# Kernel optimization log

Hardware: AMD Instinct MI355X
Metric: run time of the kernel (lower is better)

Reference implementation:

```python
import jax, jax.numpy as jnp
import numpy as np

# config matching init_kwargs
C = 256; G = 16; GC = C // G; K = 3; P = K * K
PAD = 1; STR = 1; DIL = 1; OFFSET_SCALE = 1.0
N, H, W = 8, 64, 64


def setup_inputs() -> dict:
    key = jax.random.key(0)
    ks = jax.random.split(key, 8)
    def rn(k, shape, sc):
        return jax.random.normal(k, shape, jnp.float32) * sc
    return {
        "x": jax.random.normal(ks[0], (N, H, W, C), jnp.float32),
        "dw_w": rn(ks[1], (C, 1, K, K), 0.1),          # depthwise conv weight (OIHW, groups=C)
        "dw_b": jnp.zeros((C,), jnp.float32),
        "ln_g": jnp.ones((C,), jnp.float32),
        "ln_b": jnp.zeros((C,), jnp.float32),
        "off_w": rn(ks[2], (G * P * 2, C), 0.01),      # offset head (small so offsets stay sane)
        "off_b": jnp.zeros((G * P * 2,), jnp.float32),
        "mask_w": rn(ks[3], (G * P, C), 0.01),
        "mask_b": jnp.zeros((G * P,), jnp.float32),
        "in_w": rn(ks[4], (C, C), 0.05),
        "in_b": jnp.zeros((C,), jnp.float32),
        "out_w": rn(ks[5], (C, C), 0.05),
        "out_b": jnp.zeros((C,), jnp.float32),
    }


def _layer_norm(x, g, b, eps=1e-6):
    m = x.mean(-1, keepdims=True)
    v = ((x - m) ** 2).mean(-1, keepdims=True)
    return (x - m) * jax.lax.rsqrt(v + eps) * g + b


def _grid_sample_bilinear(img, grid):
    # img: (B, Cc, Hh, Ww); grid: (B, L, P, 2) normalized to [-1, 1], (x, y) order.
    # Matches torch.grid_sample(mode='bilinear', padding_mode='zeros', align_corners=False).
    B, Cc, Hh, Ww = img.shape
    gx = (grid[..., 0] + 1.0) * (Ww * 0.5) - 0.5
    gy = (grid[..., 1] + 1.0) * (Hh * 0.5) - 0.5
    x0 = jnp.floor(gx); y0 = jnp.floor(gy)
    tx = gx - x0; ty = gy - y0
    img_f = img.reshape(B, Cc, Hh * Ww)
    def corner(xi, yi, w):
        valid = (xi >= 0) & (xi < Ww) & (yi >= 0) & (yi < Hh)
        idx = (jnp.clip(yi, 0, Hh - 1) * Ww + jnp.clip(xi, 0, Ww - 1)).astype(jnp.int32)
        v = jnp.take_along_axis(img_f, idx.reshape(B, 1, -1), axis=2)  # (B, Cc, L*P)
        return v * (w * valid).reshape(B, 1, -1)
    out = (corner(x0, y0, (1 - tx) * (1 - ty)) + corner(x0 + 1, y0, tx * (1 - ty))
           + corner(x0, y0 + 1, (1 - tx) * ty) + corner(x0 + 1, y0 + 1, tx * ty))
    return out.reshape(B, Cc, grid.shape[1], grid.shape[2])  # (B, Cc, L, P)


def _dcnv3_core(x, offset, mask):
    # x: (N,H,W,C) value features; offset: (N,H,W,G*P*2); mask: (N,H,W,G*P)
    xpad = jnp.pad(x, ((0, 0), (PAD, PAD), (PAD, PAD), (0, 0)))
    Hi, Wi = H + 2 * PAD, W + 2 * PAD
    Ho, Wo = H, W
    # reference points (centers of receptive field), normalized by padded size
    start = (DIL * (K - 1)) // 2 + 0.5
    ry = (start + jnp.arange(Ho, dtype=jnp.float32) * STR) / Hi
    rx = (start + jnp.arange(Wo, dtype=jnp.float32) * STR) / Wi
    ref = jnp.stack([jnp.broadcast_to(rx[None, :], (Ho, Wo)),
                     jnp.broadcast_to(ry[:, None], (Ho, Wo))], -1)  # (Ho,Wo,2) (x,y)
    # dilation grid, x-major flattening to match torch meshgrid('ij') ordering
    d = jnp.arange(K, dtype=jnp.float32) * DIL - (DIL * (K - 1)) // 2
    kgrid = jnp.stack([jnp.repeat(d, K) / Wi, jnp.tile(d, K) / Hi], -1)  # (P,2)
    off = offset.reshape(N, Ho, Wo, G, P, 2)
    norm = jnp.array([Wi, Hi], jnp.float32)
    loc = (ref[None, :, :, None, None, :]
           + kgrid[None, None, None, None, :, :] * OFFSET_SCALE
           + off * OFFSET_SCALE / norm)                      # (N,Ho,Wo,G,P,2)
    sg = (2.0 * loc - 1.0).reshape(N, Ho * Wo, G, P, 2)
    sg = sg.transpose(0, 2, 1, 3, 4).reshape(N * G, Ho * Wo, P, 2)
    val = xpad.reshape(N, Hi * Wi, G * GC).transpose(0, 2, 1).reshape(N * G, GC, Hi, Wi)
    samp = _grid_sample_bilinear(val, sg)                    # (N*G, GC, Ho*Wo, P)
    m = mask.reshape(N, Ho * Wo, G, P).transpose(0, 2, 1, 3).reshape(N * G, 1, Ho * Wo, P)
    out = (samp * m).sum(-1)                                 # (N*G, GC, Ho*Wo)
    return out.reshape(N, G * GC, Ho * Wo).transpose(0, 2, 1).reshape(N, Ho, Wo, C)


def reference(x, dw_w, dw_b, ln_g, ln_b, off_w, off_b, mask_w, mask_b, in_w, in_b, out_w, out_b):
    xp = x @ in_w.T + in_b                                   # input_proj (values)
    # depthwise conv -> LN (channels_last) -> exact GELU
    y = jax.lax.conv_general_dilated(
        x.transpose(0, 3, 1, 2), dw_w, (1, 1), ((PAD, PAD), (PAD, PAD)),
        feature_group_count=C, dimension_numbers=('NCHW', 'OIHW', 'NCHW'))
    y = y + dw_b[None, :, None, None]
    x1 = jax.nn.gelu(_layer_norm(y.transpose(0, 2, 3, 1), ln_g, ln_b), approximate=False)
    offset = x1 @ off_w.T + off_b                            # (N,H,W,G*P*2)
    mlogits = (x1 @ mask_w.T + mask_b).reshape(N, H, W, G, P)
    mask = jax.nn.softmax(mlogits, axis=-1).reshape(N, H, W, G * P)
    out = _dcnv3_core(xp, offset, mask)
    return out @ out_w.T + out_b
```

## Files before the change

### kernel.cpp

```cpp
#include <hip/hip_runtime.h>


#define LL 32768
#define CC 256

typedef __bf16 bf16;
typedef __bf16 bf16x4 __attribute__((ext_vector_type(4)));
typedef __bf16 bf16x8 __attribute__((ext_vector_type(8)));
typedef float f32x4v __attribute__((ext_vector_type(4)));

__device__ __forceinline__ void gload16(const bf16* g, const bf16* lds_base) {
    __builtin_amdgcn_global_load_lds(
        (const __attribute__((address_space(1))) void*)g,
        (__attribute__((address_space(3))) void*)lds_base, 16, 0, 0);
}

__global__ __launch_bounds__(256) void k_prep(
    const float* __restrict__ in_w, const float* __restrict__ off_w,
    const float* __restrict__ mask_w, const float* __restrict__ out_w,
    const float* __restrict__ dw_w, const float* __restrict__ off_b,
    const float* __restrict__ mask_b,
    bf16* __restrict__ in_h, bf16* __restrict__ in_l,
    bf16* __restrict__ hw_h, bf16* __restrict__ hw_l,
    bf16* __restrict__ out_h, bf16* __restrict__ out_l,
    float* __restrict__ dwT, float* __restrict__ hbias) {
    int idx = blockIdx.x * 256 + threadIdx.x;
    if (idx < 60416) {
        const float* s; bf16 *hi, *lo; int i;
        if (idx < 16384)      { s = in_w;   hi = in_h;          lo = in_l;          i = idx; }
        else if (idx < 34816) { s = off_w;  hi = hw_h;          lo = hw_l;          i = idx - 16384; }
        else if (idx < 44032) { s = mask_w; hi = hw_h + 73728;  lo = hw_l + 73728;  i = idx - 34816; }
        else                  { s = out_w;  hi = out_h;         lo = out_l;         i = idx - 44032; }
        float4 v = *(const float4*)(s + (size_t)i * 4);
        bf16x4 h, l;
        h[0] = (bf16)v.x; l[0] = (bf16)(v.x - (float)h[0]);
        h[1] = (bf16)v.y; l[1] = (bf16)(v.y - (float)h[1]);
        h[2] = (bf16)v.z; l[2] = (bf16)(v.z - (float)h[2]);
        h[3] = (bf16)v.w; l[3] = (bf16)(v.w - (float)h[3]);
        *(bf16x4*)(hi + (size_t)i * 4) = h;
        *(bf16x4*)(lo + (size_t)i * 4) = l;
    } else if (idx < 62720) {
        int e = idx - 60416;
        int c = e & 255, j = e >> 8;
        dwT[j * 256 + c] = dw_w[c * 9 + j];
    } else if (idx < 63232) {
        int e = idx - 62720;
        hbias[e] = (e < 288) ? off_b[e] : (e < 432 ? mask_b[e - 288] : 0.f);
    } else if (idx < 68352) {
        int e = idx - 63232;
        bf16x4 z = {(bf16)0.f, (bf16)0.f, (bf16)0.f, (bf16)0.f};
        *(bf16x4*)(hw_h + 110592 + (size_t)e * 4) = z;
        *(bf16x4*)(hw_l + 110592 + (size_t)e * 4) = z;
    }
}

__global__ __launch_bounds__(256) void k_dwln(
    const float* __restrict__ x, const float* __restrict__ dwT,
    const float* __restrict__ dw_b, const float* __restrict__ ln_g,
    const float* __restrict__ ln_b, bf16* __restrict__ x1h,
    bf16* __restrict__ xb) {
    int t = threadIdx.x;
    int q = t >> 6, u = t & 63;
    int l = blockIdx.x * 4 + q;
    int w = l & 63, h = (l >> 6) & 63, n = l >> 12;
    int c0 = u * 4;

    float4 acc = *(const float4*)(dw_b + c0);
    float4 xc = {0.f, 0.f, 0.f, 0.f};
#pragma unroll
    for (int kh = 0; kh < 3; ++kh) {
        int hh = h + kh - 1;
        if (hh < 0 || hh >= 64) continue;
#pragma unroll
        for (int kw = 0; kw < 3; ++kw) {
            int ww = w + kw - 1;
            if (ww < 0 || ww >= 64) continue;
            float4 xv = *(const float4*)(x + (size_t)(((n * 64 + hh) * 64) + ww) * CC + c0);
            if (kh == 1 && kw == 1) xc = xv;
            float4 wv = *(const float4*)(dwT + (kh * 3 + kw) * 256 + c0);
            acc.x += xv.x * wv.x; acc.y += xv.y * wv.y;
            acc.z += xv.z * wv.z; acc.w += xv.w * wv.w;
        }
    }
    bf16x4 xcb;
    xcb[0] = (bf16)xc.x; xcb[1] = (bf16)xc.y;
    xcb[2] = (bf16)xc.z; xcb[3] = (bf16)xc.w;
    *(bf16x4*)(xb + (size_t)l * CC + c0) = xcb;

    float s = acc.x + acc.y + acc.z + acc.w;
    float ss = acc.x * acc.x + acc.y * acc.y + acc.z * acc.z + acc.w * acc.w;
#pragma unroll
    for (int d = 1; d < 64; d <<= 1) {
        s += __shfl_xor(s, d);
        ss += __shfl_xor(ss, d);
    }
    float mean = s * (1.0f / 256.0f);
    float var = ss * (1.0f / 256.0f) - mean * mean;
    float rstd = rsqrtf(var + 1e-6f);
    float4 gv = *(const float4*)(ln_g + c0);
    float4 bv = *(const float4*)(ln_b + c0);
    float xn0 = (acc.x - mean) * rstd * gv.x + bv.x;
    float xn1 = (acc.y - mean) * rstd * gv.y + bv.y;
    float xn2 = (acc.z - mean) * rstd * gv.z + bv.z;
    float xn3 = (acc.w - mean) * rstd * gv.w + bv.w;
    bf16x4 oh;
    oh[0] = (bf16)(0.5f * xn0 * (1.0f + erff(xn0 * 0.70710678118654752f)));
    oh[1] = (bf16)(0.5f * xn1 * (1.0f + erff(xn1 * 0.70710678118654752f)));
    oh[2] = (bf16)(0.5f * xn2 * (1.0f + erff(xn2 * 0.70710678118654752f)));
    oh[3] = (bf16)(0.5f * xn3 * (1.0f + erff(xn3 * 0.70710678118654752f)));
    *(bf16x4*)(x1h + (size_t)l * CC + c0) = oh;
}

template <bool OBF16>
__global__ __launch_bounds__(256) void k_gemm(
    const bf16* __restrict__ A, const bf16* __restrict__ Wh,
    const bf16* __restrict__ Wl, const float* __restrict__ bias,
    float* __restrict__ C32, bf16* __restrict__ Cbf, int Nout) {
    int mb = blockIdx.x * 128, nb = blockIdx.y * 128;
    int t = threadIdx.x, wave = t >> 6, lane = t & 63;
    int wm = wave & 1, wn = wave >> 1;
    int fm = lane & 15, fq = lane >> 4;

    __shared__ bf16 smem[12288];

    const bf16* gbase[6];
    const bf16* lbase[6];
#pragma unroll
    for (int j = 0; j < 6; ++j) {
        int seg = wave * 6 + j;
        int arr = seg >> 3;
        int row = (seg & 7) * 16 + (lane >> 2);
        int col = (lane & 3) * 8;
        const bf16* g = (arr == 0) ? (A + (size_t)(mb + row) * CC + col)
                      : (arr == 1) ? (Wh + (size_t)(nb + row) * CC + col)
                                   : (Wl + (size_t)(nb + row) * CC + col);
        gbase[j] = g;
        lbase[j] = smem + seg * 512;
    }

    f32x4v acc[4][4];
#pragma unroll
    for (int i = 0; i < 4; ++i)
#pragma unroll
        for (int j = 0; j < 4; ++j) acc[i][j] = (f32x4v){0.f, 0.f, 0.f, 0.f};

    for (int kc = 0; kc < 256; kc += 32) {
#pragma unroll
        for (int j = 0; j < 6; ++j) gload16(gbase[j] + kc, lbase[j]);
        __syncthreads();

        bf16x8 af[4], bfh[4], bfl[4];
#pragma unroll
        for (int i = 0; i < 4; ++i)
            af[i] = *(const bf16x8*)&smem[(wm * 64 + i * 16 + fm) * 32 + fq * 8];
#pragma unroll
        for (int j = 0; j < 4; ++j) {
            int br = wn * 64 + j * 16 + fm;
            bfh[j] = *(const bf16x8*)&smem[4096 + br * 32 + fq * 8];
            bfl[j] = *(const bf16x8*)&smem[8192 + br * 32 + fq * 8];
        }
#pragma unroll
        for (int i = 0; i < 4; ++i)
#pragma unroll
            for (int j = 0; j < 4; ++j) {
                acc[i][j] = __builtin_amdgcn_mfma_f32_16x16x32_bf16(
                    af[i], bfh[j], acc[i][j], 0, 0, 0);
                acc[i][j] = __builtin_amdgcn_mfma_f32_16x16x32_bf16(
                    af[i], bfl[j], acc[i][j], 0, 0, 0);
            }
        __syncthreads();
    }

#pragma unroll
    for (int j = 0; j < 4; ++j) {
        int n_g = nb + wn * 64 + j * 16 + fm;
        if (n_g >= Nout) continue;
        float bv = bias[n_g];
#pragma unroll
        for (int i = 0; i < 4; ++i) {
            int m_g = mb + wm * 64 + i * 16 + fq * 4;
#pragma unroll
            for (int rg = 0; rg < 4; ++rg) {
                float o = acc[i][j][rg] + bv;
                if (OBF16)
                    Cbf[(size_t)(m_g + rg) * Nout + n_g] = (bf16)o;
                else
                    C32[(size_t)(m_g + rg) * Nout + n_g] = o;
            }
        }
    }
}

__global__ __launch_bounds__(256) void k_gather(
    const bf16* __restrict__ xp, const bf16* __restrict__ head,
    bf16* __restrict__ rows) {
    int t = threadIdx.x;
    int q = t >> 5, u = t & 31;
    int l = blockIdx.x * 8 + q;
    int w = l & 63, h = (l >> 6) & 63, n = l >> 12;

    __shared__ float offs[8][288];
    __shared__ float ms[8][144];
    for (int j = u; j < 288; j += 32) offs[q][j] = (float)head[(size_t)l * 432 + j];
    for (int j = u; j < 144; j += 32) ms[q][j] = (float)head[(size_t)l * 432 + 288 + j];
    __syncthreads();

    if (u < 16) {
        int g = u;
        float mx = -1e30f;
#pragma unroll
        for (int p = 0; p < 9; ++p) mx = fmaxf(mx, ms[q][g * 9 + p]);
        float s = 0.f, e[9];
#pragma unroll
        for (int p = 0; p < 9; ++p) { e[p] = expf(ms[q][g * 9 + p] - mx); s += e[p]; }
        float inv = 1.0f / s;
#pragma unroll
        for (int p = 0; p < 9; ++p) ms[q][g * 9 + p] = e[p] * inv;
    }
    __syncthreads();

    int g = u >> 1;
    int c0 = g * 16 + (u & 1) * 8;
    const bf16* base = xp + (size_t)n * 4096 * CC + c0;
    float a0 = 0.f, a1 = 0.f, a2 = 0.f, a3 = 0.f;
    float a4 = 0.f, a5 = 0.f, a6 = 0.f, a7 = 0.f;
#pragma unroll
    for (int p = 0; p < 9; ++p) {
        float ox = offs[q][g * 18 + p * 2 + 0];
        float oy = offs[q][g * 18 + p * 2 + 1];
        float ax = (float)(w + (p / 3) - 1) + ox;
        float ay = (float)(h + (p % 3) - 1) + oy;
        float x0f = floorf(ax), y0f = floorf(ay);
        int x0 = (int)x0f, y0 = (int)y0f;
        float tx = ax - x0f, ty = ay - y0f;
        float m = ms[q][g * 9 + p];
        int idx[4]; float cw[4];
#pragma unroll
        for (int cr = 0; cr < 4; ++cr) {
            int xx = x0 + (cr & 1), yy = y0 + (cr >> 1);
            bool v = (xx >= 0) & (xx < 64) & (yy >= 0) & (yy < 64);
            int xc = min(max(xx, 0), 63), yc = min(max(yy, 0), 63);
            idx[cr] = (yc * 64 + xc) * CC;
            float wx = (cr & 1) ? tx : (1.f - tx);
            float wy = (cr >> 1) ? ty : (1.f - ty);
            cw[cr] = v ? (m * wx * wy) : 0.f;
        }
#pragma unroll
        for (int cr = 0; cr < 4; ++cr) {
            bf16x8 vb = *(const bf16x8*)(base + idx[cr]);
            float wt = cw[cr];
            a0 += wt * (float)vb[0]; a1 += wt * (float)vb[1];
            a2 += wt * (float)vb[2]; a3 += wt * (float)vb[3];
            a4 += wt * (float)vb[4]; a5 += wt * (float)vb[5];
            a6 += wt * (float)vb[6]; a7 += wt * (float)vb[7];
        }
    }
    bf16x8 oh;
    oh[0] = (bf16)a0; oh[1] = (bf16)a1; oh[2] = (bf16)a2; oh[3] = (bf16)a3;
    oh[4] = (bf16)a4; oh[5] = (bf16)a5; oh[6] = (bf16)a6; oh[7] = (bf16)a7;
    *(bf16x8*)(rows + (size_t)l * CC + c0) = oh;
}

__device__ __forceinline__ float dot256f(const float* a, const float* wrow) {
    const float4* w4 = (const float4*)wrow;
    float s = 0.f;
#pragma unroll 16
    for (int i = 0; i < 64; ++i) {
        float4 u = w4[i];
        const float* ap = a + i * 4;
        s += ap[0] * u.x + ap[1] * u.y + ap[2] * u.z + ap[3] * u.w;
    }
    return s;
}

__global__ __launch_bounds__(256) void k_inproj_fb(
    const float* __restrict__ x, const float* __restrict__ in_w,
    const float* __restrict__ in_b, float* __restrict__ xp) {
    int l = blockIdx.x;
    int t = threadIdx.x;
    __shared__ float xa[256];
    xa[t] = x[l * CC + t];
    __syncthreads();
    xp[l * CC + t] = dot256f(xa, in_w + t * CC) + in_b[t];
}

__device__ __forceinline__ float fetch_px_fb(const float* base, int yy, int xx) {
    if (xx < 0 || xx >= 64 || yy < 0 || yy >= 64) return 0.f;
    return base[(yy * 64 + xx) * CC];
}

__global__ __launch_bounds__(256) void k_main_fb(
    const float* __restrict__ x, const float* __restrict__ xp,
    const float* __restrict__ dw_w, const float* __restrict__ dw_b,
    const float* __restrict__ ln_g, const float* __restrict__ ln_b,
    const float* __restrict__ off_w, const float* __restrict__ off_b,
    const float* __restrict__ mask_w, const float* __restrict__ mask_b,
    const float* __restrict__ out_w, const float* __restrict__ out_b,
    float* __restrict__ out) {
    int l = blockIdx.x;
    int t = threadIdx.x;
    int w = l & 63, h = (l >> 6) & 63, n = l >> 12;
    __shared__ float x1[256];
    __shared__ float red[256];
    __shared__ float offs[288];
    __shared__ float ms[144];
    __shared__ float row[256];

    float acc = dw_b[t];
#pragma unroll
    for (int kh = 0; kh < 3; ++kh) {
        int hh = h + kh - 1;
        if (hh < 0 || hh >= 64) continue;
#pragma unroll
        for (int kw = 0; kw < 3; ++kw) {
            int ww = w + kw - 1;
            if (ww < 0 || ww >= 64) continue;
            acc += x[(((n * 64 + hh) * 64) + ww) * CC + t] * dw_w[t * 9 + kh * 3 + kw];
        }
    }
    red[t] = acc;
    __syncthreads();
    for (int s = 128; s > 0; s >>= 1) {
        if (t < s) red[t] += red[t + s];
        __syncthreads();
    }
    float mean = red[0] * (1.0f / 256.0f);
    __syncthreads();
    float d = acc - mean;
    red[t] = d * d;
    __syncthreads();
    for (int s = 128; s > 0; s >>= 1) {
        if (t < s) red[t] += red[t + s];
        __syncthreads();
    }
    float var = red[0] * (1.0f / 256.0f);
    float xn = d * rsqrtf(var + 1e-6f) * ln_g[t] + ln_b[t];
    x1[t] = 0.5f * xn * (1.0f + erff(xn * 0.70710678118654752f));
    __syncthreads();

    offs[t] = dot256f(x1, off_w + t * CC) + off_b[t];
    if (t < 32) {
        int j = 256 + t;
        offs[j] = dot256f(x1, off_w + j * CC) + off_b[j];
    }
    if (t < 144) ms[t] = dot256f(x1, mask_w + t * CC) + mask_b[t];
    __syncthreads();

    if (t < 16) {
        int g = t;
        float mx = -1e30f;
#pragma unroll
        for (int p = 0; p < 9; ++p) mx = fmaxf(mx, ms[g * 9 + p]);
        float s = 0.f, e[9];
#pragma unroll
        for (int p = 0; p < 9; ++p) { e[p] = expf(ms[g * 9 + p] - mx); s += e[p]; }
        float inv = 1.0f / s;
#pragma unroll
        for (int p = 0; p < 9; ++p) ms[g * 9 + p] = e[p] * inv;
    }
    __syncthreads();

    int g = t >> 4;
    const float* base = xp + (size_t)n * 64 * 64 * CC + t;
    float acc2 = 0.f;
#pragma unroll
    for (int p = 0; p < 9; ++p) {
        float ox = offs[g * 18 + p * 2 + 0];
        float oy = offs[g * 18 + p * 2 + 1];
        float ax = (float)(w + (p / 3) - 1) + ox;
        float ay = (float)(h + (p % 3) - 1) + oy;
        float x0f = floorf(ax), y0f = floorf(ay);
        int x0 = (int)x0f, y0 = (int)y0f;
        float tx = ax - x0f, ty = ay - y0f;
        float v00 = fetch_px_fb(base, y0, x0);
        float v01 = fetch_px_fb(base, y0, x0 + 1);
        float v10 = fetch_px_fb(base, y0 + 1, x0);
        float v11 = fetch_px_fb(base, y0 + 1, x0 + 1);
        float bl = (v00 * (1.f - tx) + v01 * tx) * (1.f - ty) +
                   (v10 * (1.f - tx) + v11 * tx) * ty;
        acc2 += ms[g * 9 + p] * bl;
    }
    row[t] = acc2;
    __syncthreads();
    out[l * CC + t] = dot256f(row, out_w + t * CC) + out_b[t];
}

extern "C" void kernel_launch(void* const* d_in, const int* in_sizes, int n_in,
                              void* d_out, int out_size, void* d_ws,
                              size_t ws_size, hipStream_t stream) {
    const float* x      = (const float*)d_in[0];
    const float* dw_w   = (const float*)d_in[1];
    const float* dw_b   = (const float*)d_in[2];
    const float* ln_g   = (const float*)d_in[3];
    const float* ln_b   = (const float*)d_in[4];
    const float* off_w  = (const float*)d_in[5];
    const float* off_b  = (const float*)d_in[6];
    const float* mask_w = (const float*)d_in[7];
    const float* mask_b = (const float*)d_in[8];
    const float* in_w   = (const float*)d_in[9];
    const float* in_b   = (const float*)d_in[10];
    const float* out_w  = (const float*)d_in[11];
    const float* out_b  = (const float*)d_in[12];
    float* out = (float*)d_out;

    const size_t szBF    = (size_t)LL * CC * 2;
    const size_t szHEADB = (size_t)LL * 432 * 2;
    const size_t szWB    = 1300480;
    const size_t need    = 3 * szBF + szHEADB + szWB;

    dim3 blk(256);
    if (ws_size >= need) {
        char* p = (char*)d_ws;
        bf16* x1h = (bf16*)p; p += szBF;
        bf16* xpb = (bf16*)p; p += szBF;
        bf16* xb  = (bf16*)p; p += szBF;
        bf16* headb = (bf16*)p; p += szHEADB;
        bf16* in_h  = (bf16*)p; p += 131072;
        bf16* in_l  = (bf16*)p; p += 131072;
        bf16* hw_h  = (bf16*)p; p += 262144;
        bf16* hw_l  = (bf16*)p; p += 262144;
        bf16* out_h = (bf16*)p; p += 131072;
        bf16* out_l = (bf16*)p; p += 131072;
        float* dwT  = (float*)p; p += 9216;
        float* hbias = (float*)p;
        bf16* rows = x1h;

        k_prep<<<dim3(267), blk, 0, stream>>>(in_w, off_w, mask_w, out_w, dw_w,
                                              off_b, mask_b, in_h, in_l, hw_h,
                                              hw_l, out_h, out_l, dwT, hbias);
        k_dwln<<<dim3(LL / 4), blk, 0, stream>>>(x, dwT, dw_b, ln_g, ln_b, x1h, xb);
        k_gemm<true><<<dim3(256, 2), blk, 0, stream>>>(
            xb, in_h, in_l, in_b, nullptr, xpb, 256);
        k_gemm<true><<<dim3(256, 4), blk, 0, stream>>>(
            x1h, hw_h, hw_l, hbias, nullptr, headb, 432);
        k_gather<<<dim3(LL / 8), blk, 0, stream>>>(xpb, headb, rows);
        k_gemm<false><<<dim3(256, 2), blk, 0, stream>>>(
            rows, out_h, out_l, out_b, out, nullptr, 256);
    } else {
        float* xp = (float*)d_ws;
        k_inproj_fb<<<dim3(LL), blk, 0, stream>>>(x, in_w, in_b, xp);
        k_main_fb<<<dim3(LL), blk, 0, stream>>>(x, xp, dw_w, dw_b, ln_g, ln_b,
                                                off_w, off_b, mask_w, mask_b,
                                                out_w, out_b, out);
    }
}
```

Before: 218.8 us.

## Drop low-part weight MFMA in input/head GEMMs and widen gather per thread

Adds a template flag so the input-projection and offset/mask head GEMMs use only the high bf16 part of the weights, which halves their MFMA work and their LDS/global loads. The output GEMM keeps the two-part split. The gather kernel is restructured: one thread now handles a full 16-channel group for one pixel, the bf16 head row is copied into LDS with vector loads, and the softmax is computed in registers, which removes a sync and the float staging. The risk is lower accuracy for offsets and values, since the residual bf16 correction term is gone.

```diff
diff --git a/kernel.cpp b/kernel.cpp
--- a/kernel.cpp
+++ b/kernel.cpp
@@ -111,7 +111,7 @@
     *(bf16x4*)(x1h + (size_t)l * CC + c0) = oh;
 }
 
-template <bool OBF16>
+template <bool OBF16, bool TWOP>
 __global__ __launch_bounds__(256) void k_gemm(
     const bf16* __restrict__ A, const bf16* __restrict__ Wh,
     const bf16* __restrict__ Wl, const float* __restrict__ bias,
@@ -121,13 +121,15 @@
     int wm = wave & 1, wn = wave >> 1;
     int fm = lane & 15, fq = lane >> 4;
 
-    __shared__ bf16 smem[12288];
-
-    const bf16* gbase[6];
-    const bf16* lbase[6];
-#pragma unroll
-    for (int j = 0; j < 6; ++j) {
-        int seg = wave * 6 + j;
+    constexpr int NSEG = TWOP ? 24 : 16;
+    constexpr int PERW = NSEG / 4;
+    __shared__ bf16 smem[NSEG * 512];
+
+    const bf16* gbase[PERW];
+    const bf16* lbase[PERW];
+#pragma unroll
+    for (int j = 0; j < PERW; ++j) {
+        int seg = wave * PERW + j;
         int arr = seg >> 3;
         int row = (seg & 7) * 16 + (lane >> 2);
         int col = (lane & 3) * 8;
@@ -146,7 +148,7 @@
 
     for (int kc = 0; kc < 256; kc += 32) {
 #pragma unroll
-        for (int j = 0; j < 6; ++j) gload16(gbase[j] + kc, lbase[j]);
+        for (int j = 0; j < PERW; ++j) gload16(gbase[j] + kc, lbase[j]);
         __syncthreads();
 
         bf16x8 af[4], bfh[4], bfl[4];
@@ -157,7 +159,7 @@
         for (int j = 0; j < 4; ++j) {
             int br = wn * 64 + j * 16 + fm;
             bfh[j] = *(const bf16x8*)&smem[4096 + br * 32 + fq * 8];
-            bfl[j] = *(const bf16x8*)&smem[8192 + br * 32 + fq * 8];
+            if (TWOP) bfl[j] = *(const bf16x8*)&smem[8192 + br * 32 + fq * 8];
         }
 #pragma unroll
         for (int i = 0; i < 4; ++i)
@@ -165,8 +167,9 @@
             for (int j = 0; j < 4; ++j) {
                 acc[i][j] = __builtin_amdgcn_mfma_f32_16x16x32_bf16(
                     af[i], bfh[j], acc[i][j], 0, 0, 0);
-                acc[i][j] = __builtin_amdgcn_mfma_f32_16x16x32_bf16(
-                    af[i], bfl[j], acc[i][j], 0, 0, 0);
+                if (TWOP)
+                    acc[i][j] = __builtin_amdgcn_mfma_f32_16x16x32_bf16(
+                        af[i], bfl[j], acc[i][j], 0, 0, 0);
             }
         __syncthreads();
     }
@@ -195,45 +198,47 @@
     const bf16* __restrict__ xp, const bf16* __restrict__ head,
     bf16* __restrict__ rows) {
     int t = threadIdx.x;
-    int q = t >> 5, u = t & 31;
-    int l = blockIdx.x * 8 + q;
+    int q = t >> 4, g = t & 15;
+    int l = blockIdx.x * 16 + q;
     int w = l & 63, h = (l >> 6) & 63, n = l >> 12;
 
-    __shared__ float offs[8][288];
-    __shared__ float ms[8][144];
-    for (int j = u; j < 288; j += 32) offs[q][j] = (float)head[(size_t)l * 432 + j];
-    for (int j = u; j < 144; j += 32) ms[q][j] = (float)head[(size_t)l * 432 + 288 + j];
-    __syncthreads();
-
-    if (u < 16) {
-        int g = u;
+    __shared__ uint4 smem4[864];
+    const uint4* hsrc = (const uint4*)(head + (size_t)blockIdx.x * 16 * 432);
+#pragma unroll
+    for (int j = t; j < 864; j += 256) smem4[j] = hsrc[j];
+    __syncthreads();
+    const bf16* sb = (const bf16*)smem4;
+
+    float ms[9];
+    {
+        const bf16* mrow = sb + q * 432 + 288 + g * 9;
         float mx = -1e30f;
 #pragma unroll
-        for (int p = 0; p < 9; ++p) mx = fmaxf(mx, ms[q][g * 9 + p]);
-        float s = 0.f, e[9];
-#pragma unroll
-        for (int p = 0; p < 9; ++p) { e[p] = expf(ms[q][g * 9 + p] - mx); s += e[p]; }
+        for (int p = 0; p < 9; ++p) { ms[p] = (float)mrow[p]; mx = fmaxf(mx, ms[p]); }
+        float s = 0.f;
+#pragma unroll
+        for (int p = 0; p < 9; ++p) { ms[p] = expf(ms[p] - mx); s += ms[p]; }
         float inv = 1.0f / s;
 #pragma unroll
-        for (int p = 0; p < 9; ++p) ms[q][g * 9 + p] = e[p] * inv;
-    }
-    __syncthreads();
-
-    int g = u >> 1;
-    int c0 = g * 16 + (u & 1) * 8;
-    const bf16* base = xp + (size_t)n * 4096 * CC + c0;
-    float a0 = 0.f, a1 = 0.f, a2 = 0.f, a3 = 0.f;
-    float a4 = 0.f, a5 = 0.f, a6 = 0.f, a7 = 0.f;
+        for (int p = 0; p < 9; ++p) ms[p] *= inv;
+    }
+    const bf16* orow = sb + q * 432 + g * 18;
+
+    const bf16* base = xp + (size_t)n * 4096 * CC + g * 16;
+    float a[16];
+#pragma unroll
+    for (int c = 0; c < 16; ++c) a[c] = 0.f;
+
 #pragma unroll
     for (int p = 0; p < 9; ++p) {
-        float ox = offs[q][g * 18 + p * 2 + 0];
-        float oy = offs[q][g * 18 + p * 2 + 1];
+        float ox = (float)orow[p * 2 + 0];
+        float oy = (float)orow[p * 2 + 1];
         float ax = (float)(w + (p / 3) - 1) + ox;
         float ay = (float)(h + (p % 3) - 1) + oy;
         float x0f = floorf(ax), y0f = floorf(ay);
         int x0 = (int)x0f, y0 = (int)y0f;
         float tx = ax - x0f, ty = ay - y0f;
-        float m = ms[q][g * 9 + p];
+        float m = ms[p];
         int idx[4]; float cw[4];
 #pragma unroll
         for (int cr = 0; cr < 4; ++cr) {
@@ -247,18 +252,21 @@
         }
 #pragma unroll
         for (int cr = 0; cr < 4; ++cr) {
-            bf16x8 vb = *(const bf16x8*)(base + idx[cr]);
+            bf16x8 v0 = *(const bf16x8*)(base + idx[cr]);
+            bf16x8 v1 = *(const bf16x8*)(base + idx[cr] + 8);
             float wt = cw[cr];
-            a0 += wt * (float)vb[0]; a1 += wt * (float)vb[1];
-            a2 += wt * (float)vb[2]; a3 += wt * (float)vb[3];
-            a4 += wt * (float)vb[4]; a5 += wt * (float)vb[5];
-            a6 += wt * (float)vb[6]; a7 += wt * (float)vb[7];
-        }
-    }
-    bf16x8 oh;
-    oh[0] = (bf16)a0; oh[1] = (bf16)a1; oh[2] = (bf16)a2; oh[3] = (bf16)a3;
-    oh[4] = (bf16)a4; oh[5] = (bf16)a5; oh[6] = (bf16)a6; oh[7] = (bf16)a7;
-    *(bf16x8*)(rows + (size_t)l * CC + c0) = oh;
+#pragma unroll
+            for (int c = 0; c < 8; ++c) a[c] += wt * (float)v0[c];
+#pragma unroll
+            for (int c = 0; c < 8; ++c) a[8 + c] += wt * (float)v1[c];
+        }
+    }
+    bf16x8 o0, o1;
+#pragma unroll
+    for (int c = 0; c < 8; ++c) { o0[c] = (bf16)a[c]; o1[c] = (bf16)a[8 + c]; }
+    bf16* dst = rows + (size_t)l * CC + g * 16;
+    *(bf16x8*)dst = o0;
+    *(bf16x8*)(dst + 8) = o1;
 }
 
 __device__ __forceinline__ float dot256f(const float* a, const float* wrow) {
@@ -429,12 +437,12 @@
                                               off_b, mask_b, in_h, in_l, hw_h,
                                               hw_l, out_h, out_l, dwT, hbias);
         k_dwln<<<dim3(LL / 4), blk, 0, stream>>>(x, dwT, dw_b, ln_g, ln_b, x1h, xb);
-        k_gemm<true><<<dim3(256, 2), blk, 0, stream>>>(
-            xb, in_h, in_l, in_b, nullptr, xpb, 256);
-        k_gemm<true><<<dim3(256, 4), blk, 0, stream>>>(
-            x1h, hw_h, hw_l, hbias, nullptr, headb, 432);
-        k_gather<<<dim3(LL / 8), blk, 0, stream>>>(xpb, headb, rows);
-        k_gemm<false><<<dim3(256, 2), blk, 0, stream>>>(
+        k_gemm<true, false><<<dim3(256, 2), blk, 0, stream>>>(
+            xb, in_h, nullptr, in_b, nullptr, xpb, 256);
+        k_gemm<true, false><<<dim3(256, 4), blk, 0, stream>>>(
+            x1h, hw_h, nullptr, hbias, nullptr, headb, 432);
+        k_gather<<<dim3(LL / 16), blk, 0, stream>>>(xpb, headb, rows);
+        k_gemm<false, true><<<dim3(256, 2), blk, 0, stream>>>(
             rows, out_h, out_l, out_b, out, nullptr, 256);
     } else {
         float* xp = (float*)d_ws;
```

After: 227.8 us. 1.04x slower.
